# Kernel tuning notes

Measured on AMD Instinct MI355X. Metric: run time of the kernel, lower is better.

Reference implementation:

```python
import jax, jax.numpy as jnp
import numpy as np
from jax import lax

D_TEMPORAL, D_INNER, D_STATE, D_CONV, DT_RANK = 2, 4, 16, 4, 1
EPS = 1e-5


def setup_inputs() -> dict:
    key = jax.random.key(0)
    ks = jax.random.split(key, 14)
    B, L = 16, 32768
    f = lambda k, s, scale=1.0: jax.random.normal(k, s, jnp.float32) * scale
    dt_b = float(np.log(np.expm1(0.01)))  # softplus^-1(0.01), typical dt init
    A_log = jnp.log(jnp.tile(jnp.arange(1, D_STATE + 1, dtype=jnp.float32), (D_INNER, 1)))
    return {
        "hidden_states": f(ks[0], (B, D_TEMPORAL, L)),
        "norm_w": jnp.ones((D_TEMPORAL,), jnp.float32),
        "in_proj_w": f(ks[1], (2 * D_INNER, D_TEMPORAL), 0.5),
        "conv_w": f(ks[2], (D_INNER, D_CONV), 0.3),
        "conv_b": f(ks[3], (D_INNER,), 0.1),
        "x_proj_w": f(ks[4], (DT_RANK + 2 * D_STATE, D_INNER), 0.3),
        "dt_proj_w": f(ks[5], (D_INNER, DT_RANK), 1.0),
        "dt_proj_b": jnp.full((D_INNER,), dt_b, jnp.float32),
        "A_log": A_log,
        "D": jnp.ones((D_INNER,), jnp.float32),
        "conv_w_b": f(ks[6], (D_INNER, D_CONV), 0.3),
        "conv_b_b": f(ks[7], (D_INNER,), 0.1),
        "x_proj_w_b": f(ks[8], (DT_RANK + 2 * D_STATE, D_INNER), 0.3),
        "dt_proj_w_b": f(ks[9], (D_INNER, DT_RANK), 1.0),
        "dt_proj_b_b": jnp.full((D_INNER,), dt_b, jnp.float32),
        "A_b_log": A_log,
        "D_b": jnp.ones((D_INNER,), jnp.float32),
        "out_proj_w": f(ks[10], (D_TEMPORAL, D_INNER), 0.3),
        "norm_f_w": jnp.ones((D_TEMPORAL,), jnp.float32),
    }


def _silu(x):
    return x * jax.nn.sigmoid(x)


def _rmsnorm(x, w):
    return x * lax.rsqrt(jnp.mean(x * x, axis=-1, keepdims=True) + EPS) * w


def _branch(x, z, conv_w, conv_b, x_proj_w, dt_proj_w, dt_proj_b, A_log, D):
    # x, z: (B, d_inner, L). Causal depthwise conv + silu.
    Bb, d, L = x.shape
    xc = lax.conv_general_dilated(
        x, conv_w[:, None, :], (1,), [(D_CONV - 1, 0)],
        feature_group_count=d, dimension_numbers=("NCH", "OIH", "NCH"))
    u = _silu(xc + conv_b[None, :, None]).transpose(0, 2, 1)      # (B, L, d)
    x_dbl = u @ x_proj_w.T                                        # (B, L, rank+2n)
    dt, Bm, Cm = jnp.split(x_dbl, [DT_RANK, DT_RANK + D_STATE], axis=-1)
    dt = jax.nn.softplus(dt @ dt_proj_w.T + dt_proj_b)            # (B, L, d)
    A = -jnp.exp(A_log)                                           # (d, n)
    dA = jnp.exp(dt[..., None] * A)                               # (B, L, d, n)
    dBu = (dt * u)[..., None] * Bm[:, :, None, :]                 # (B, L, d, n)

    def step(h, inp):
        dA_t, dBu_t, C_t = inp
        h = dA_t * h + dBu_t                                      # (B, d, n)
        return h, jnp.einsum("bdn,bn->bd", h, C_t)

    h0 = jnp.zeros((Bb, d, D_STATE), dtype=u.dtype)
    _, ys = lax.scan(step, h0, (jnp.swapaxes(dA, 0, 1), jnp.swapaxes(dBu, 0, 1), jnp.swapaxes(Cm, 0, 1)))
    y = jnp.swapaxes(ys, 0, 1) + u * D                            # (B, L, d)
    return y * _silu(z.transpose(0, 2, 1))


def _forward(hidden_states, norm_w, in_proj_w, conv_w, conv_b, x_proj_w, dt_proj_w,
             dt_proj_b, A_log, D, conv_w_b, conv_b_b, x_proj_w_b, dt_proj_w_b,
             dt_proj_b_b, A_b_log, D_b, out_proj_w, norm_f_w):
    # hidden_states: (B, T=d_temporal, L); scan runs over L.
    hs = jnp.swapaxes(hidden_states, 1, 2)                        # (B, L, T)
    residual = hs.astype(jnp.float32)
    hs = _rmsnorm(residual, norm_w)
    xz = jnp.swapaxes(hs @ in_proj_w.T, 1, 2)                     # (B, 2*d_inner, L)
    x, z = jnp.split(xz, 2, axis=1)
    y_f = _branch(x, z, conv_w, conv_b, x_proj_w, dt_proj_w, dt_proj_b, A_log, D)
    y_b = _branch(x[..., ::-1], z[..., ::-1], conv_w_b, conv_b_b, x_proj_w_b,
                  dt_proj_w_b, dt_proj_b_b, A_b_log, D_b)
    y = y_f + y_b[:, ::-1, :]                                     # (B, L, d_inner)
    out = y @ out_proj_w.T                                        # (B, L, T)
    out = _rmsnorm(out + residual, norm_f_w)
    return jnp.swapaxes(out, 1, 2)                                # (B, T, L)


def reference(hidden_states, norm_w, in_proj_w, conv_w, conv_b, x_proj_w, dt_proj_w,
              dt_proj_b, A_log, D, conv_w_b, conv_b_b, x_proj_w_b, dt_proj_w_b,
              dt_proj_b_b, A_b_log, D_b, out_proj_w, norm_f_w):
    return _forward(hidden_states, norm_w, in_proj_w, conv_w, conv_b, x_proj_w,
                    dt_proj_w, dt_proj_b, A_log, D, conv_w_b, conv_b_b, x_proj_w_b,
                    dt_proj_w_b, dt_proj_b_b, A_b_log, D_b, out_proj_w, norm_f_w)
```

## Files before the change

### kernel.cpp

```cpp
#include <hip/hip_runtime.h>
#include <cstdint>

#define BB 16
#define LL 32768
#define NC 512

#define WD_SZ 256
#define XPW 0
#define CVW 132
#define CVB 148
#define DTW 152
#define DTB 156
#define AW  160
#define DW  224
#define G_INPROJ 512
#define G_NORMW 528
#define G_OUTP 530
#define G_NORMF 538
#define FLG 1000

#define PQ_OFF 4096
#define PQ_BYTES ((size_t)BB*2*NC*64*8)
#define HIN_OFF (PQ_OFF + PQ_BYTES)

__device__ __forceinline__ float bf2f(unsigned short u){ return __uint_as_float(((unsigned int)u)<<16); }
__device__ __forceinline__ float blo(unsigned int u){ return __uint_as_float(u<<16); }
__device__ __forceinline__ float bhi(unsigned int u){ return __uint_as_float(u & 0xffff0000u); }
__device__ __forceinline__ unsigned short f2bf(float f){
  unsigned int x = __float_as_uint(f);
  x += 0x7fffu + ((x>>16)&1u);
  return (unsigned short)(x>>16);
}
__device__ __forceinline__ unsigned int pack2(float a, float b){
  return (unsigned int)f2bf(a) | ((unsigned int)f2bf(b)<<16);
}
__device__ __forceinline__ float siluf(float x){ return x / (1.f + __expf(-x)); }
__device__ __forceinline__ float softplusf_(float x){ return fmaxf(x,0.f) + log1pf(__expf(-fabsf(x))); }

__device__ __forceinline__ float rowsum16(float x){
  union { float f; int i; } a, t;
  a.f = x;
  t.i = __builtin_amdgcn_update_dpp(0, a.i, 0x121, 0xf, 0xf, true); a.f += t.f;
  t.i = __builtin_amdgcn_update_dpp(0, a.i, 0x122, 0xf, 0xf, true); a.f += t.f;
  t.i = __builtin_amdgcn_update_dpp(0, a.i, 0x124, 0xf, 0xf, true); a.f += t.f;
  t.i = __builtin_amdgcn_update_dpp(0, a.i, 0x128, 0xf, 0xf, true); a.f += t.f;
  return a.f;
}

__device__ __forceinline__ float ldw(const void* p, int i, int isf){
  return isf ? ((const float*)p)[i] : bf2f(((const unsigned short*)p)[i]);
}
__device__ __forceinline__ float2 hid2(const void* hid, int isf, int b, int t){
  if (isf){
    const float* p = (const float*)hid;
    return make_float2(p[(size_t)b*2*LL + t], p[(size_t)b*2*LL + LL + t]);
  }
  const unsigned short* p = (const unsigned short*)hid;
  return make_float2(bf2f(p[(size_t)b*2*LL + t]), bf2f(p[(size_t)b*2*LL + LL + t]));
}
__device__ __forceinline__ float4 xrow(const void* __restrict__ hid, int isf,
                                       const float* __restrict__ W, int b, int t){
  float2 h = hid2(hid, isf, b, t);
  float ms = rsqrtf(0.5f*(h.x*h.x + h.y*h.y) + 1e-5f);
  float v0 = h.x*ms*W[G_NORMW], v1 = h.y*ms*W[G_NORMW+1];
  float4 x;
  x.x = W[G_INPROJ+0]*v0 + W[G_INPROJ+1]*v1;
  x.y = W[G_INPROJ+2]*v0 + W[G_INPROJ+3]*v1;
  x.z = W[G_INPROJ+4]*v0 + W[G_INPROJ+5]*v1;
  x.w = W[G_INPROJ+6]*v0 + W[G_INPROJ+7]*v1;
  return x;
}

__global__ void k_prep(const void* __restrict__ normw, const void* __restrict__ inpj,
    const void* __restrict__ cwf, const void* __restrict__ cbf,
    const void* __restrict__ xpf, const void* __restrict__ dwf,
    const void* __restrict__ dbf, const void* __restrict__ alf,
    const void* __restrict__ ddf,
    const void* __restrict__ cwb, const void* __restrict__ cbb,
    const void* __restrict__ xpb, const void* __restrict__ dwb,
    const void* __restrict__ dbb, const void* __restrict__ alb,
    const void* __restrict__ ddb,
    const void* __restrict__ outp, const void* __restrict__ nfw,
    float* __restrict__ W)
{
  const int isf = (((const unsigned int*)ddf)[0] == 0x3F800000u) ? 1 : 0;
  int t = threadIdx.x;
  for (int i=t;i<132;i+=256){ W[XPW+i]=ldw(xpf,i,isf); W[WD_SZ+XPW+i]=ldw(xpb,i,isf); }
  for (int i=t;i<16;i+=256){ W[CVW+i]=ldw(cwf,i,isf); W[WD_SZ+CVW+i]=ldw(cwb,i,isf); W[G_INPROJ+i]=ldw(inpj,i,isf); }
  for (int i=t;i<4;i+=256){
    W[CVB+i]=ldw(cbf,i,isf); W[WD_SZ+CVB+i]=ldw(cbb,i,isf);
    W[DTW+i]=ldw(dwf,i,isf); W[WD_SZ+DTW+i]=ldw(dwb,i,isf);
    W[DTB+i]=ldw(dbf,i,isf); W[WD_SZ+DTB+i]=ldw(dbb,i,isf);
    W[DW+i] =ldw(ddf,i,isf); W[WD_SZ+DW+i] =ldw(ddb,i,isf);
  }
  for (int i=t;i<64;i+=256){ W[AW+i] = -__expf(ldw(alf,i,isf)); W[WD_SZ+AW+i] = -__expf(ldw(alb,i,isf)); }
  for (int i=t;i<8;i+=256) W[G_OUTP+i]=ldw(outp,i,isf);
  for (int i=t;i<2;i+=256){ W[G_NORMW+i]=ldw(normw,i,isf); W[G_NORMF+i]=ldw(nfw,i,isf); }
  if (t==0) W[FLG] = (float)isf;
}

__global__ __launch_bounds__(64) void k_chunk(const void* __restrict__ hid,
    const float* __restrict__ W, float2* __restrict__ PQ)
{
  __shared__ __align__(16) float4 xb[70];
  __shared__ __align__(16) float dtP[2][4][68];
  __shared__ __align__(16) unsigned short dtuP[2][4][72];
  __shared__ __align__(16) unsigned short Bp[2][16][72];
  const int lane = threadIdx.x;
  const int gid  = blockIdx.x;
  const int c    = gid & (NC-1);
  const int b    = gid >> 9;
  const int isf  = (int)W[FLG];

  {
    int t = c*64 + lane;
    xb[lane+3] = xrow(hid, isf, W, b, t);
    if (lane < 3){
      int t2 = c*64 - 3 + lane;
      float4 v = make_float4(0.f,0.f,0.f,0.f);
      if (t2 >= 0) v = xrow(hid, isf, W, b, t2);
      xb[lane] = v;
    }
    if (lane >= 61){
      int t3 = c*64 + lane + 3;
      float4 v = make_float4(0.f,0.f,0.f,0.f);
      if (t3 < LL) v = xrow(hid, isf, W, b, t3);
      xb[lane+6] = v;
    }
  }
  __syncthreads();
  {
    float4 xk0=xb[lane],xk1=xb[lane+1],xk2=xb[lane+2],xk3=xb[lane+3];
    float4 xk4=xb[lane+4],xk5=xb[lane+5],xk6=xb[lane+6];
    float uf[4], ub[4];
    uf[0] = siluf(W[CVB+0] + W[CVW+ 0]*xk0.x + W[CVW+ 1]*xk1.x + W[CVW+ 2]*xk2.x + W[CVW+ 3]*xk3.x);
    uf[1] = siluf(W[CVB+1] + W[CVW+ 4]*xk0.y + W[CVW+ 5]*xk1.y + W[CVW+ 6]*xk2.y + W[CVW+ 7]*xk3.y);
    uf[2] = siluf(W[CVB+2] + W[CVW+ 8]*xk0.z + W[CVW+ 9]*xk1.z + W[CVW+10]*xk2.z + W[CVW+11]*xk3.z);
    uf[3] = siluf(W[CVB+3] + W[CVW+12]*xk0.w + W[CVW+13]*xk1.w + W[CVW+14]*xk2.w + W[CVW+15]*xk3.w);
    const float* Wb = W + WD_SZ;
    ub[0] = siluf(Wb[CVB+0] + Wb[CVW+ 0]*xk6.x + Wb[CVW+ 1]*xk5.x + Wb[CVW+ 2]*xk4.x + Wb[CVW+ 3]*xk3.x);
    ub[1] = siluf(Wb[CVB+1] + Wb[CVW+ 4]*xk6.y + Wb[CVW+ 5]*xk5.y + Wb[CVW+ 6]*xk4.y + Wb[CVW+ 7]*xk3.y);
    ub[2] = siluf(Wb[CVB+2] + Wb[CVW+ 8]*xk6.z + Wb[CVW+ 9]*xk5.z + Wb[CVW+10]*xk4.z + Wb[CVW+11]*xk3.z);
    ub[3] = siluf(Wb[CVB+3] + Wb[CVW+12]*xk6.w + Wb[CVW+13]*xk5.w + Wb[CVW+14]*xk4.w + Wb[CVW+15]*xk3.w);
    #pragma unroll
    for (int dr=0; dr<2; dr++){
      const float* Wd = W + dr*WD_SZ;
      const float* uu = dr ? ub : uf;
      float dtr = Wd[XPW+0]*uu[0] + Wd[XPW+1]*uu[1] + Wd[XPW+2]*uu[2] + Wd[XPW+3]*uu[3];
      #pragma unroll
      for (int d2=0; d2<4; d2++){
        float dt = softplusf_(fmaf(Wd[DTW+d2], dtr, Wd[DTB+d2]));
        dtP[dr][d2][lane]  = dt;
        dtuP[dr][d2][lane] = f2bf(dt*uu[d2]);
      }
      #pragma unroll
      for (int n=0; n<16; n++){
        float Bn = Wd[XPW+(1+n)*4+0]*uu[0] + Wd[XPW+(1+n)*4+1]*uu[1]
                 + Wd[XPW+(1+n)*4+2]*uu[2] + Wd[XPW+(1+n)*4+3]*uu[3];
        Bp[dr][n][lane] = f2bf(Bn);
      }
    }
  }
  __syncthreads();
  const int d = lane>>4, n = lane&15;
  const float Af = W[AW + d*16 + n];
  const float Ab = W[WD_SZ + AW + d*16 + n];
  float Pf=1.f, Qf=0.f, Pb=1.f, Qb=0.f;
  for (int j4=0; j4<16; j4++){
    const int t0f = j4*4, t0b = 60 - j4*4;
    float4 df4 = *(const float4*)&dtP[0][d][t0f];
    float4 db4 = *(const float4*)&dtP[1][d][t0b];
    ushort4 uf4 = *(const ushort4*)&dtuP[0][d][t0f];
    ushort4 ub4 = *(const ushort4*)&dtuP[1][d][t0b];
    ushort4 bf4 = *(const ushort4*)&Bp[0][n][t0f];
    ushort4 bb4 = *(const ushort4*)&Bp[1][n][t0b];
    float dfa[4]={df4.x,df4.y,df4.z,df4.w}, dba[4]={db4.x,db4.y,db4.z,db4.w};
    unsigned short ufa[4]={uf4.x,uf4.y,uf4.z,uf4.w}, uba[4]={ub4.x,ub4.y,ub4.z,ub4.w};
    unsigned short bfa[4]={bf4.x,bf4.y,bf4.z,bf4.w}, bba[4]={bb4.x,bb4.y,bb4.z,bb4.w};
    #pragma unroll
    for (int jr=0; jr<4; jr++){
      float e = __expf(Af*dfa[jr]);
      Pf *= e;
      Qf = fmaf(Qf, e, bf2f(ufa[jr])*bf2f(bfa[jr]));
      const int k = 3-jr;
      float eb = __expf(Ab*dba[k]);
      Pb *= eb;
      Qb = fmaf(Qb, eb, bf2f(uba[k])*bf2f(bba[k]));
    }
  }
  PQ[((size_t)(b*2+0)*NC + c)*64 + lane]          = make_float2(Pf,Qf);
  PQ[((size_t)(b*2+1)*NC + (NC-1-c))*64 + lane]   = make_float2(Pb,Qb);
}

__global__ __launch_bounds__(64) void k_scan(const float2* __restrict__ PQ, float* __restrict__ hin)
{
  int bd = blockIdx.x; int lane = threadIdx.x;
  float h = 0.f;
  size_t base = (size_t)bd*NC;
  for (int c0=0; c0<NC; c0+=16){
    float2 v[16];
    #pragma unroll
    for (int k=0;k<16;k++) v[k] = PQ[(base+c0+k)*64 + lane];
    #pragma unroll
    for (int k=0;k<16;k++){
      hin[(base+c0+k)*64 + lane] = h;
      h = fmaf(v[k].x, h, v[k].y);
    }
  }
}

__global__ __launch_bounds__(64) void k_fused(const void* __restrict__ hid,
    const float* __restrict__ W, const float* __restrict__ hin,
    void* __restrict__ out)
{
  __shared__ __align__(16) float4 xb[70];
  __shared__ __align__(16) float dtP[2][4][68];
  __shared__ __align__(16) unsigned short dtuP[2][4][72];
  __shared__ __align__(16) unsigned int BCp[2][16][68];
  __shared__ __align__(16) float ySf[4][68];
  __shared__ __align__(16) float ySb[4][68];
  __shared__ __align__(16) float zs[256];
  __shared__ __align__(16) float uD2[2][256];
  const int lane = threadIdx.x;
  const int gid  = blockIdx.x;
  const int c    = gid & (NC-1);
  const int b    = gid >> 9;
  const int isf  = (int)W[FLG];

  float hF = hin[((size_t)(b*2+0)*NC + c)*64 + lane];
  float hB = hin[((size_t)(b*2+1)*NC + (NC-1-c))*64 + lane];

  {
    int t = c*64 + lane;
    float2 h = hid2(hid, isf, b, t);
    float ms = rsqrtf(0.5f*(h.x*h.x + h.y*h.y) + 1e-5f);
    float v0 = h.x*ms*W[G_NORMW], v1 = h.y*ms*W[G_NORMW+1];
    float4 x;
    x.x = W[G_INPROJ+0]*v0 + W[G_INPROJ+1]*v1;
    x.y = W[G_INPROJ+2]*v0 + W[G_INPROJ+3]*v1;
    x.z = W[G_INPROJ+4]*v0 + W[G_INPROJ+5]*v1;
    x.w = W[G_INPROJ+6]*v0 + W[G_INPROJ+7]*v1;
    xb[lane+3] = x;
    float4 z4;
    z4.x = siluf(W[G_INPROJ+ 8]*v0 + W[G_INPROJ+ 9]*v1);
    z4.y = siluf(W[G_INPROJ+10]*v0 + W[G_INPROJ+11]*v1);
    z4.z = siluf(W[G_INPROJ+12]*v0 + W[G_INPROJ+13]*v1);
    z4.w = siluf(W[G_INPROJ+14]*v0 + W[G_INPROJ+15]*v1);
    *(float4*)&zs[lane*4] = z4;
    if (lane < 3){
      int t2 = c*64 - 3 + lane;
      float4 v = make_float4(0.f,0.f,0.f,0.f);
      if (t2 >= 0) v = xrow(hid, isf, W, b, t2);
      xb[lane] = v;
    }
    if (lane >= 61){
      int t3 = c*64 + lane + 3;
      float4 v = make_float4(0.f,0.f,0.f,0.f);
      if (t3 < LL) v = xrow(hid, isf, W, b, t3);
      xb[lane+6] = v;
    }
  }
  __syncthreads();
  {
    float4 xk0=xb[lane],xk1=xb[lane+1],xk2=xb[lane+2],xk3=xb[lane+3];
    float4 xk4=xb[lane+4],xk5=xb[lane+5],xk6=xb[lane+6];
    float uf[4], ub[4];
    uf[0] = siluf(W[CVB+0] + W[CVW+ 0]*xk0.x + W[CVW+ 1]*xk1.x + W[CVW+ 2]*xk2.x + W[CVW+ 3]*xk3.x);
    uf[1] = siluf(W[CVB+1] + W[CVW+ 4]*xk0.y + W[CVW+ 5]*xk1.y + W[CVW+ 6]*xk2.y + W[CVW+ 7]*xk3.y);
    uf[2] = siluf(W[CVB+2] + W[CVW+ 8]*xk0.z + W[CVW+ 9]*xk1.z + W[CVW+10]*xk2.z + W[CVW+11]*xk3.z);
    uf[3] = siluf(W[CVB+3] + W[CVW+12]*xk0.w + W[CVW+13]*xk1.w + W[CVW+14]*xk2.w + W[CVW+15]*xk3.w);
    const float* Wb = W + WD_SZ;
    ub[0] = siluf(Wb[CVB+0] + Wb[CVW+ 0]*xk6.x + Wb[CVW+ 1]*xk5.x + Wb[CVW+ 2]*xk4.x + Wb[CVW+ 3]*xk3.x);
    ub[1] = siluf(Wb[CVB+1] + Wb[CVW+ 4]*xk6.y + Wb[CVW+ 5]*xk5.y + Wb[CVW+ 6]*xk4.y + Wb[CVW+ 7]*xk3.y);
    ub[2] = siluf(Wb[CVB+2] + Wb[CVW+ 8]*xk6.z + Wb[CVW+ 9]*xk5.z + Wb[CVW+10]*xk4.z + Wb[CVW+11]*xk3.z);
    ub[3] = siluf(Wb[CVB+3] + Wb[CVW+12]*xk6.w + Wb[CVW+13]*xk5.w + Wb[CVW+14]*xk4.w + Wb[CVW+15]*xk3.w);
    #pragma unroll
    for (int dr=0; dr<2; dr++){
      const float* Wd = W + dr*WD_SZ;
      const float* uu = dr ? ub : uf;
      float dtr = Wd[XPW+0]*uu[0] + Wd[XPW+1]*uu[1] + Wd[XPW+2]*uu[2] + Wd[XPW+3]*uu[3];
      float4 ud4;
      #pragma unroll
      for (int d2=0; d2<4; d2++){
        float dt = softplusf_(fmaf(Wd[DTW+d2], dtr, Wd[DTB+d2]));
        dtP[dr][d2][lane]  = dt;
        dtuP[dr][d2][lane] = f2bf(dt*uu[d2]);
        ((float*)&ud4)[d2] = uu[d2]*Wd[DW+d2];
      }
      *(float4*)&uD2[dr][lane*4] = ud4;
      #pragma unroll
      for (int n=0; n<16; n++){
        float Bn = Wd[XPW+(1+n)*4+0]*uu[0] + Wd[XPW+(1+n)*4+1]*uu[1]
                 + Wd[XPW+(1+n)*4+2]*uu[2] + Wd[XPW+(1+n)*4+3]*uu[3];
        float Cn = Wd[XPW+(17+n)*4+0]*uu[0] + Wd[XPW+(17+n)*4+1]*uu[1]
                 + Wd[XPW+(17+n)*4+2]*uu[2] + Wd[XPW+(17+n)*4+3]*uu[3];
        BCp[dr][n][lane] = pack2(Bn, Cn);
      }
    }
  }
  __syncthreads();

  const int d = lane>>4, n = lane&15;
  const float Af = W[AW + d*16 + n];
  const float Ab = W[WD_SZ + AW + d*16 + n];
  for (int j4=0; j4<16; j4++){
    const int t0f = j4*4, t0b = 60 - j4*4;
    float4 df4 = *(const float4*)&dtP[0][d][t0f];
    float4 db4 = *(const float4*)&dtP[1][d][t0b];
    ushort4 uf4 = *(const ushort4*)&dtuP[0][d][t0f];
    ushort4 ub4 = *(const ushort4*)&dtuP[1][d][t0b];
    uint4 cf4 = *(const uint4*)&BCp[0][n][t0f];
    uint4 cb4 = *(const uint4*)&BCp[1][n][t0b];
    float dfa[4]={df4.x,df4.y,df4.z,df4.w}, dba[4]={db4.x,db4.y,db4.z,db4.w};
    unsigned short ufa[4]={uf4.x,uf4.y,uf4.z,uf4.w}, uba[4]={ub4.x,ub4.y,ub4.z,ub4.w};
    unsigned int cfa[4]={cf4.x,cf4.y,cf4.z,cf4.w}, cba[4]={cb4.x,cb4.y,cb4.z,cb4.w};
    float sF[4], sB[4];
    #pragma unroll
    for (int jr=0; jr<4; jr++){
      float e = __expf(Af*dfa[jr]);
      hF = fmaf(e, hF, bf2f(ufa[jr])*blo(cfa[jr]));
      sF[jr] = rowsum16(hF*bhi(cfa[jr]));
      const int k = 3-jr;
      float eb = __expf(Ab*dba[k]);
      hB = fmaf(eb, hB, bf2f(uba[k])*blo(cba[k]));
      sB[k] = rowsum16(hB*bhi(cba[k]));
    }
    if (n == 0){
      *(float4*)&ySf[d][t0f] = make_float4(sF[0],sF[1],sF[2],sF[3]);
      *(float4*)&ySb[d][t0b] = make_float4(sB[0],sB[1],sB[2],sB[3]);
    }
  }
  __syncthreads();

  {
    int t = c*64 + lane;
    float4 zz = *(const float4*)&zs[lane*4];
    float4 u0 = *(const float4*)&uD2[0][lane*4];
    float4 u1 = *(const float4*)&uD2[1][lane*4];
    float y0 = (ySf[0][lane] + ySb[0][lane] + u0.x + u1.x) * zz.x;
    float y1 = (ySf[1][lane] + ySb[1][lane] + u0.y + u1.y) * zz.y;
    float y2 = (ySf[2][lane] + ySb[2][lane] + u0.z + u1.z) * zz.z;
    float y3 = (ySf[3][lane] + ySb[3][lane] + u0.w + u1.w) * zz.w;
    float o0 = W[G_OUTP+0]*y0 + W[G_OUTP+1]*y1 + W[G_OUTP+2]*y2 + W[G_OUTP+3]*y3;
    float o1 = W[G_OUTP+4]*y0 + W[G_OUTP+5]*y1 + W[G_OUTP+6]*y2 + W[G_OUTP+7]*y3;
    float2 r = hid2(hid, isf, b, t);
    o0 += r.x;
    o1 += r.y;
    float ms = rsqrtf(0.5f*(o0*o0 + o1*o1) + 1e-5f);
    float e0 = o0*ms*W[G_NORMF], e1 = o1*ms*W[G_NORMF+1];
    size_t i0 = (size_t)b*2*LL + t, i1 = i0 + LL;
    if (isf){
      ((float*)out)[i0] = e0;
      ((float*)out)[i1] = e1;
    } else {
      ((unsigned short*)out)[i0] = f2bf(e0);
      ((unsigned short*)out)[i1] = f2bf(e1);
    }
  }
}

extern "C" void kernel_launch(void* const* d_in, const int* in_sizes, int n_in,
                              void* d_out, int out_size, void* d_ws, size_t ws_size,
                              hipStream_t stream)
{
  (void)in_sizes; (void)n_in; (void)out_size; (void)ws_size;
  const void* hid   = d_in[0];
  const void* normw = d_in[1];
  const void* inpj  = d_in[2];
  const void* cwf   = d_in[3];
  const void* cbf   = d_in[4];
  const void* xpf   = d_in[5];
  const void* dwf   = d_in[6];
  const void* dbf   = d_in[7];
  const void* alf   = d_in[8];
  const void* ddf   = d_in[9];
  const void* cwb   = d_in[10];
  const void* cbb   = d_in[11];
  const void* xpb   = d_in[12];
  const void* dwb   = d_in[13];
  const void* dbb   = d_in[14];
  const void* alb   = d_in[15];
  const void* ddb   = d_in[16];
  const void* outp  = d_in[17];
  const void* nfw   = d_in[18];

  float* W   = (float*)d_ws;
  float2* PQ = (float2*)((char*)d_ws + PQ_OFF);
  float* hin = (float*)((char*)d_ws + HIN_OFF);

  k_prep<<<1,256,0,stream>>>(normw, inpj, cwf, cbf, xpf, dwf, dbf, alf, ddf,
                             cwb, cbb, xpb, dwb, dbb, alb, ddb, outp, nfw, W);
  k_chunk<<<BB*NC, 64, 0, stream>>>(hid, W, PQ);
  k_scan<<<BB*2, 64, 0, stream>>>(PQ, hin);
  k_fused<<<BB*NC, 64, 0, stream>>>(hid, W, hin, d_out);
}
```

Baseline: 206.9 us.

## Share precomputed chunk planes between passes and split the carry scan across four waves

The chunk pass now writes its per-chunk dt, dt*u, packed B/C, z and D*u planes to workspace, so the fused pass can load them instead of recomputing conv, projections and activations. This applies only when the workspace is large enough; otherwise both passes recompute as before. The carry scan now runs four waves per sequence, each over its own segment, then corrects the carries with the prefix of the earlier segments. Silu and softplus use cheaper hardware rcp and log2 intrinsics. The cost is about 109 MB of extra global write and read traffic.

```diff
diff --git a/kernel.cpp b/kernel.cpp
--- a/kernel.cpp
+++ b/kernel.cpp
@@ -22,6 +22,11 @@
 #define PQ_OFF 4096
 #define PQ_BYTES ((size_t)BB*2*NC*64*8)
 #define HIN_OFF (PQ_OFF + PQ_BYTES)
+#define HIN_BYTES ((size_t)BB*2*NC*64*4)
+#define PLN_OFF (HIN_OFF + HIN_BYTES)
+#define PLN_STRIDE 13312
+#define PLN_BYTES ((size_t)BB*NC*PLN_STRIDE)
+
 
 __device__ __forceinline__ float bf2f(unsigned short u){ return __uint_as_float(((unsigned int)u)<<16); }
 __device__ __forceinline__ float blo(unsigned int u){ return __uint_as_float(u<<16); }
@@ -34,8 +39,12 @@
 __device__ __forceinline__ unsigned int pack2(float a, float b){
   return (unsigned int)f2bf(a) | ((unsigned int)f2bf(b)<<16);
 }
-__device__ __forceinline__ float siluf(float x){ return x / (1.f + __expf(-x)); }
-__device__ __forceinline__ float softplusf_(float x){ return fmaxf(x,0.f) + log1pf(__expf(-fabsf(x))); }
+__device__ __forceinline__ float siluf(float x){
+  return x * __builtin_amdgcn_rcpf(1.f + __expf(-x));
+}
+__device__ __forceinline__ float softplusf_(float x){
+  return fmaxf(x,0.f) + 0.69314718056f*__log2f(1.f + __expf(-fabsf(x)));
+}
 
 __device__ __forceinline__ float rowsum16(float x){
   union { float f; int i; } a, t;
@@ -71,165 +80,18 @@
   return x;
 }
 
-__global__ void k_prep(const void* __restrict__ normw, const void* __restrict__ inpj,
-    const void* __restrict__ cwf, const void* __restrict__ cbf,
-    const void* __restrict__ xpf, const void* __restrict__ dwf,
-    const void* __restrict__ dbf, const void* __restrict__ alf,
-    const void* __restrict__ ddf,
-    const void* __restrict__ cwb, const void* __restrict__ cbb,
-    const void* __restrict__ xpb, const void* __restrict__ dwb,
-    const void* __restrict__ dbb, const void* __restrict__ alb,
-    const void* __restrict__ ddb,
-    const void* __restrict__ outp, const void* __restrict__ nfw,
-    float* __restrict__ W)
-{
-  const int isf = (((const unsigned int*)ddf)[0] == 0x3F800000u) ? 1 : 0;
-  int t = threadIdx.x;
-  for (int i=t;i<132;i+=256){ W[XPW+i]=ldw(xpf,i,isf); W[WD_SZ+XPW+i]=ldw(xpb,i,isf); }
-  for (int i=t;i<16;i+=256){ W[CVW+i]=ldw(cwf,i,isf); W[WD_SZ+CVW+i]=ldw(cwb,i,isf); W[G_INPROJ+i]=ldw(inpj,i,isf); }
-  for (int i=t;i<4;i+=256){
-    W[CVB+i]=ldw(cbf,i,isf); W[WD_SZ+CVB+i]=ldw(cbb,i,isf);
-    W[DTW+i]=ldw(dwf,i,isf); W[WD_SZ+DTW+i]=ldw(dwb,i,isf);
-    W[DTB+i]=ldw(dbf,i,isf); W[WD_SZ+DTB+i]=ldw(dbb,i,isf);
-    W[DW+i] =ldw(ddf,i,isf); W[WD_SZ+DW+i] =ldw(ddb,i,isf);
-  }
-  for (int i=t;i<64;i+=256){ W[AW+i] = -__expf(ldw(alf,i,isf)); W[WD_SZ+AW+i] = -__expf(ldw(alb,i,isf)); }
-  for (int i=t;i<8;i+=256) W[G_OUTP+i]=ldw(outp,i,isf);
-  for (int i=t;i<2;i+=256){ W[G_NORMW+i]=ldw(normw,i,isf); W[G_NORMF+i]=ldw(nfw,i,isf); }
-  if (t==0) W[FLG] = (float)isf;
-}
-
-__global__ __launch_bounds__(64) void k_chunk(const void* __restrict__ hid,
-    const float* __restrict__ W, float2* __restrict__ PQ)
-{
-  __shared__ __align__(16) float4 xb[70];
-  __shared__ __align__(16) float dtP[2][4][68];
-  __shared__ __align__(16) unsigned short dtuP[2][4][72];
-  __shared__ __align__(16) unsigned short Bp[2][16][72];
-  const int lane = threadIdx.x;
-  const int gid  = blockIdx.x;
-  const int c    = gid & (NC-1);
-  const int b    = gid >> 9;
-  const int isf  = (int)W[FLG];
-
-  {
-    int t = c*64 + lane;
-    xb[lane+3] = xrow(hid, isf, W, b, t);
-    if (lane < 3){
-      int t2 = c*64 - 3 + lane;
-      float4 v = make_float4(0.f,0.f,0.f,0.f);
-      if (t2 >= 0) v = xrow(hid, isf, W, b, t2);
-      xb[lane] = v;
-    }
-    if (lane >= 61){
-      int t3 = c*64 + lane + 3;
-      float4 v = make_float4(0.f,0.f,0.f,0.f);
-      if (t3 < LL) v = xrow(hid, isf, W, b, t3);
-      xb[lane+6] = v;
-    }
-  }
-  __syncthreads();
-  {
-    float4 xk0=xb[lane],xk1=xb[lane+1],xk2=xb[lane+2],xk3=xb[lane+3];
-    float4 xk4=xb[lane+4],xk5=xb[lane+5],xk6=xb[lane+6];
-    float uf[4], ub[4];
-    uf[0] = siluf(W[CVB+0] + W[CVW+ 0]*xk0.x + W[CVW+ 1]*xk1.x + W[CVW+ 2]*xk2.x + W[CVW+ 3]*xk3.x);
-    uf[1] = siluf(W[CVB+1] + W[CVW+ 4]*xk0.y + W[CVW+ 5]*xk1.y + W[CVW+ 6]*xk2.y + W[CVW+ 7]*xk3.y);
-    uf[2] = siluf(W[CVB+2] + W[CVW+ 8]*xk0.z + W[CVW+ 9]*xk1.z + W[CVW+10]*xk2.z + W[CVW+11]*xk3.z);
-    uf[3] = siluf(W[CVB+3] + W[CVW+12]*xk0.w + W[CVW+13]*xk1.w + W[CVW+14]*xk2.w + W[CVW+15]*xk3.w);
-    const float* Wb = W + WD_SZ;
-    ub[0] = siluf(Wb[CVB+0] + Wb[CVW+ 0]*xk6.x + Wb[CVW+ 1]*xk5.x + Wb[CVW+ 2]*xk4.x + Wb[CVW+ 3]*xk3.x);
-    ub[1] = siluf(Wb[CVB+1] + Wb[CVW+ 4]*xk6.y + Wb[CVW+ 5]*xk5.y + Wb[CVW+ 6]*xk4.y + Wb[CVW+ 7]*xk3.y);
-    ub[2] = siluf(Wb[CVB+2] + Wb[CVW+ 8]*xk6.z + Wb[CVW+ 9]*xk5.z + Wb[CVW+10]*xk4.z + Wb[CVW+11]*xk3.z);
-    ub[3] = siluf(Wb[CVB+3] + Wb[CVW+12]*xk6.w + Wb[CVW+13]*xk5.w + Wb[CVW+14]*xk4.w + Wb[CVW+15]*xk3.w);
-    #pragma unroll
-    for (int dr=0; dr<2; dr++){
-      const float* Wd = W + dr*WD_SZ;
-      const float* uu = dr ? ub : uf;
-      float dtr = Wd[XPW+0]*uu[0] + Wd[XPW+1]*uu[1] + Wd[XPW+2]*uu[2] + Wd[XPW+3]*uu[3];
-      #pragma unroll
-      for (int d2=0; d2<4; d2++){
-        float dt = softplusf_(fmaf(Wd[DTW+d2], dtr, Wd[DTB+d2]));
-        dtP[dr][d2][lane]  = dt;
-        dtuP[dr][d2][lane] = f2bf(dt*uu[d2]);
-      }
-      #pragma unroll
-      for (int n=0; n<16; n++){
-        float Bn = Wd[XPW+(1+n)*4+0]*uu[0] + Wd[XPW+(1+n)*4+1]*uu[1]
-                 + Wd[XPW+(1+n)*4+2]*uu[2] + Wd[XPW+(1+n)*4+3]*uu[3];
-        Bp[dr][n][lane] = f2bf(Bn);
-      }
-    }
-  }
-  __syncthreads();
-  const int d = lane>>4, n = lane&15;
-  const float Af = W[AW + d*16 + n];
-  const float Ab = W[WD_SZ + AW + d*16 + n];
-  float Pf=1.f, Qf=0.f, Pb=1.f, Qb=0.f;
-  for (int j4=0; j4<16; j4++){
-    const int t0f = j4*4, t0b = 60 - j4*4;
-    float4 df4 = *(const float4*)&dtP[0][d][t0f];
-    float4 db4 = *(const float4*)&dtP[1][d][t0b];
-    ushort4 uf4 = *(const ushort4*)&dtuP[0][d][t0f];
-    ushort4 ub4 = *(const ushort4*)&dtuP[1][d][t0b];
-    ushort4 bf4 = *(const ushort4*)&Bp[0][n][t0f];
-    ushort4 bb4 = *(const ushort4*)&Bp[1][n][t0b];
-    float dfa[4]={df4.x,df4.y,df4.z,df4.w}, dba[4]={db4.x,db4.y,db4.z,db4.w};
-    unsigned short ufa[4]={uf4.x,uf4.y,uf4.z,uf4.w}, uba[4]={ub4.x,ub4.y,ub4.z,ub4.w};
-    unsigned short bfa[4]={bf4.x,bf4.y,bf4.z,bf4.w}, bba[4]={bb4.x,bb4.y,bb4.z,bb4.w};
-    #pragma unroll
-    for (int jr=0; jr<4; jr++){
-      float e = __expf(Af*dfa[jr]);
-      Pf *= e;
-      Qf = fmaf(Qf, e, bf2f(ufa[jr])*bf2f(bfa[jr]));
-      const int k = 3-jr;
-      float eb = __expf(Ab*dba[k]);
-      Pb *= eb;
-      Qb = fmaf(Qb, eb, bf2f(uba[k])*bf2f(bba[k]));
-    }
-  }
-  PQ[((size_t)(b*2+0)*NC + c)*64 + lane]          = make_float2(Pf,Qf);
-  PQ[((size_t)(b*2+1)*NC + (NC-1-c))*64 + lane]   = make_float2(Pb,Qb);
-}
-
-__global__ __launch_bounds__(64) void k_scan(const float2* __restrict__ PQ, float* __restrict__ hin)
-{
-  int bd = blockIdx.x; int lane = threadIdx.x;
-  float h = 0.f;
-  size_t base = (size_t)bd*NC;
-  for (int c0=0; c0<NC; c0+=16){
-    float2 v[16];
-    #pragma unroll
-    for (int k=0;k<16;k++) v[k] = PQ[(base+c0+k)*64 + lane];
-    #pragma unroll
-    for (int k=0;k<16;k++){
-      hin[(base+c0+k)*64 + lane] = h;
-      h = fmaf(v[k].x, h, v[k].y);
-    }
-  }
-}
-
-__global__ __launch_bounds__(64) void k_fused(const void* __restrict__ hid,
-    const float* __restrict__ W, const float* __restrict__ hin,
-    void* __restrict__ out)
-{
-  __shared__ __align__(16) float4 xb[70];
-  __shared__ __align__(16) float dtP[2][4][68];
-  __shared__ __align__(16) unsigned short dtuP[2][4][72];
-  __shared__ __align__(16) unsigned int BCp[2][16][68];
-  __shared__ __align__(16) float ySf[4][68];
-  __shared__ __align__(16) float ySb[4][68];
-  __shared__ __align__(16) float zs[256];
-  __shared__ __align__(16) float uD2[2][256];
-  const int lane = threadIdx.x;
-  const int gid  = blockIdx.x;
-  const int c    = gid & (NC-1);
-  const int b    = gid >> 9;
-  const int isf  = (int)W[FLG];
-
-  float hF = hin[((size_t)(b*2+0)*NC + c)*64 + lane];
-  float hB = hin[((size_t)(b*2+1)*NC + (NC-1-c))*64 + lane];
-
+__device__ __forceinline__ void phaseA(const void* __restrict__ hid, int isf,
+    const float* __restrict__ W, int b, int c, int lane,
+    unsigned char* smem, float4* xb)
+{
+  float* dtF = (float*)(smem);
+  float* dtB = (float*)(smem+1024);
+  unsigned short* duF = (unsigned short*)(smem+2048);
+  unsigned short* duB = (unsigned short*)(smem+2560);
+  unsigned int* BCF = (unsigned int*)(smem+3072);
+  unsigned int* BCB = (unsigned int*)(smem+7168);
+  float* zsP = (float*)(smem+11264);
+  float* uDP = (float*)(smem+12288);
   {
     int t = c*64 + lane;
     float2 h = hid2(hid, isf, b, t);
@@ -246,7 +108,7 @@
     z4.y = siluf(W[G_INPROJ+10]*v0 + W[G_INPROJ+11]*v1);
     z4.z = siluf(W[G_INPROJ+12]*v0 + W[G_INPROJ+13]*v1);
     z4.w = siluf(W[G_INPROJ+14]*v0 + W[G_INPROJ+15]*v1);
-    *(float4*)&zs[lane*4] = z4;
+    *(float4*)&zsP[lane*4] = z4;
     if (lane < 3){
       int t2 = c*64 - 3 + lane;
       float4 v = make_float4(0.f,0.f,0.f,0.f);
@@ -261,68 +123,237 @@
     }
   }
   __syncthreads();
-  {
-    float4 xk0=xb[lane],xk1=xb[lane+1],xk2=xb[lane+2],xk3=xb[lane+3];
-    float4 xk4=xb[lane+4],xk5=xb[lane+5],xk6=xb[lane+6];
-    float uf[4], ub[4];
-    uf[0] = siluf(W[CVB+0] + W[CVW+ 0]*xk0.x + W[CVW+ 1]*xk1.x + W[CVW+ 2]*xk2.x + W[CVW+ 3]*xk3.x);
-    uf[1] = siluf(W[CVB+1] + W[CVW+ 4]*xk0.y + W[CVW+ 5]*xk1.y + W[CVW+ 6]*xk2.y + W[CVW+ 7]*xk3.y);
-    uf[2] = siluf(W[CVB+2] + W[CVW+ 8]*xk0.z + W[CVW+ 9]*xk1.z + W[CVW+10]*xk2.z + W[CVW+11]*xk3.z);
-    uf[3] = siluf(W[CVB+3] + W[CVW+12]*xk0.w + W[CVW+13]*xk1.w + W[CVW+14]*xk2.w + W[CVW+15]*xk3.w);
-    const float* Wb = W + WD_SZ;
-    ub[0] = siluf(Wb[CVB+0] + Wb[CVW+ 0]*xk6.x + Wb[CVW+ 1]*xk5.x + Wb[CVW+ 2]*xk4.x + Wb[CVW+ 3]*xk3.x);
-    ub[1] = siluf(Wb[CVB+1] + Wb[CVW+ 4]*xk6.y + Wb[CVW+ 5]*xk5.y + Wb[CVW+ 6]*xk4.y + Wb[CVW+ 7]*xk3.y);
-    ub[2] = siluf(Wb[CVB+2] + Wb[CVW+ 8]*xk6.z + Wb[CVW+ 9]*xk5.z + Wb[CVW+10]*xk4.z + Wb[CVW+11]*xk3.z);
-    ub[3] = siluf(Wb[CVB+3] + Wb[CVW+12]*xk6.w + Wb[CVW+13]*xk5.w + Wb[CVW+14]*xk4.w + Wb[CVW+15]*xk3.w);
-    #pragma unroll
-    for (int dr=0; dr<2; dr++){
-      const float* Wd = W + dr*WD_SZ;
-      const float* uu = dr ? ub : uf;
-      float dtr = Wd[XPW+0]*uu[0] + Wd[XPW+1]*uu[1] + Wd[XPW+2]*uu[2] + Wd[XPW+3]*uu[3];
-      float4 ud4;
+  float4 xk0=xb[lane],xk1=xb[lane+1],xk2=xb[lane+2],xk3=xb[lane+3];
+  float4 xk4=xb[lane+4],xk5=xb[lane+5],xk6=xb[lane+6];
+  float uf[4], ub[4];
+  uf[0] = siluf(W[CVB+0] + W[CVW+ 0]*xk0.x + W[CVW+ 1]*xk1.x + W[CVW+ 2]*xk2.x + W[CVW+ 3]*xk3.x);
+  uf[1] = siluf(W[CVB+1] + W[CVW+ 4]*xk0.y + W[CVW+ 5]*xk1.y + W[CVW+ 6]*xk2.y + W[CVW+ 7]*xk3.y);
+  uf[2] = siluf(W[CVB+2] + W[CVW+ 8]*xk0.z + W[CVW+ 9]*xk1.z + W[CVW+10]*xk2.z + W[CVW+11]*xk3.z);
+  uf[3] = siluf(W[CVB+3] + W[CVW+12]*xk0.w + W[CVW+13]*xk1.w + W[CVW+14]*xk2.w + W[CVW+15]*xk3.w);
+  const float* Wb = W + WD_SZ;
+  ub[0] = siluf(Wb[CVB+0] + Wb[CVW+ 0]*xk6.x + Wb[CVW+ 1]*xk5.x + Wb[CVW+ 2]*xk4.x + Wb[CVW+ 3]*xk3.x);
+  ub[1] = siluf(Wb[CVB+1] + Wb[CVW+ 4]*xk6.y + Wb[CVW+ 5]*xk5.y + Wb[CVW+ 6]*xk4.y + Wb[CVW+ 7]*xk3.y);
+  ub[2] = siluf(Wb[CVB+2] + Wb[CVW+ 8]*xk6.z + Wb[CVW+ 9]*xk5.z + Wb[CVW+10]*xk4.z + Wb[CVW+11]*xk3.z);
+  ub[3] = siluf(Wb[CVB+3] + Wb[CVW+12]*xk6.w + Wb[CVW+13]*xk5.w + Wb[CVW+14]*xk4.w + Wb[CVW+15]*xk3.w);
+  *(float4*)&uDP[lane*4] = make_float4(
+      uf[0]*W[DW+0]+ub[0]*Wb[DW+0], uf[1]*W[DW+1]+ub[1]*Wb[DW+1],
+      uf[2]*W[DW+2]+ub[2]*Wb[DW+2], uf[3]*W[DW+3]+ub[3]*Wb[DW+3]);
+  #pragma unroll
+  for (int dr=0; dr<2; dr++){
+    const float* Wd = W + dr*WD_SZ;
+    const float* uu = dr ? ub : uf;
+    float* dtp = dr ? dtB : dtF;
+    unsigned short* dup = dr ? duB : duF;
+    unsigned int* bcp = dr ? BCB : BCF;
+    float dtr = Wd[XPW+0]*uu[0]+Wd[XPW+1]*uu[1]+Wd[XPW+2]*uu[2]+Wd[XPW+3]*uu[3];
+    #pragma unroll
+    for (int d2=0; d2<4; d2++){
+      float dt = softplusf_(fmaf(Wd[DTW+d2], dtr, Wd[DTB+d2]));
+      dtp[d2*64+lane] = dt;
+      dup[d2*64+lane] = f2bf(dt*uu[d2]);
+    }
+    #pragma unroll
+    for (int n=0;n<16;n++){
+      float Bn = Wd[XPW+(1+n)*4+0]*uu[0]+Wd[XPW+(1+n)*4+1]*uu[1]
+               + Wd[XPW+(1+n)*4+2]*uu[2]+Wd[XPW+(1+n)*4+3]*uu[3];
+      float Cn = Wd[XPW+(17+n)*4+0]*uu[0]+Wd[XPW+(17+n)*4+1]*uu[1]
+               + Wd[XPW+(17+n)*4+2]*uu[2]+Wd[XPW+(17+n)*4+3]*uu[3];
+      bcp[n*64+lane] = pack2(Bn,Cn);
+    }
+  }
+}
+
+__global__ void k_prep(const void* __restrict__ normw, const void* __restrict__ inpj,
+    const void* __restrict__ cwf, const void* __restrict__ cbf,
+    const void* __restrict__ xpf, const void* __restrict__ dwf,
+    const void* __restrict__ dbf, const void* __restrict__ alf,
+    const void* __restrict__ ddf,
+    const void* __restrict__ cwb, const void* __restrict__ cbb,
+    const void* __restrict__ xpb, const void* __restrict__ dwb,
+    const void* __restrict__ dbb, const void* __restrict__ alb,
+    const void* __restrict__ ddb,
+    const void* __restrict__ outp, const void* __restrict__ nfw,
+    float* __restrict__ W)
+{
+  const int isf = (((const unsigned int*)ddf)[0] == 0x3F800000u) ? 1 : 0;
+  int t = threadIdx.x;
+  for (int i=t;i<132;i+=256){ W[XPW+i]=ldw(xpf,i,isf); W[WD_SZ+XPW+i]=ldw(xpb,i,isf); }
+  for (int i=t;i<16;i+=256){ W[CVW+i]=ldw(cwf,i,isf); W[WD_SZ+CVW+i]=ldw(cwb,i,isf); W[G_INPROJ+i]=ldw(inpj,i,isf); }
+  for (int i=t;i<4;i+=256){
+    W[CVB+i]=ldw(cbf,i,isf); W[WD_SZ+CVB+i]=ldw(cbb,i,isf);
+    W[DTW+i]=ldw(dwf,i,isf); W[WD_SZ+DTW+i]=ldw(dwb,i,isf);
+    W[DTB+i]=ldw(dbf,i,isf); W[WD_SZ+DTB+i]=ldw(dbb,i,isf);
+    W[DW+i] =ldw(ddf,i,isf); W[WD_SZ+DW+i] =ldw(ddb,i,isf);
+  }
+  for (int i=t;i<64;i+=256){ W[AW+i] = -__expf(ldw(alf,i,isf)); W[WD_SZ+AW+i] = -__expf(ldw(alb,i,isf)); }
+  for (int i=t;i<8;i+=256) W[G_OUTP+i]=ldw(outp,i,isf);
+  for (int i=t;i<2;i+=256){ W[G_NORMW+i]=ldw(normw,i,isf); W[G_NORMF+i]=ldw(nfw,i,isf); }
+  if (t==0) W[FLG] = (float)isf;
+}
+
+template<bool SPL>
+__global__ __launch_bounds__(64) void k_chunk(const void* __restrict__ hid,
+    const float* __restrict__ W, float2* __restrict__ PQ,
+    unsigned char* __restrict__ planes)
+{
+  __shared__ __align__(16) unsigned char smem[13312];
+  __shared__ __align__(16) float4 xb[70];
+  const int lane = threadIdx.x;
+  const int gid  = blockIdx.x;
+  const int c    = gid & (NC-1);
+  const int b    = gid >> 9;
+  const int isf  = (int)W[FLG];
+
+  phaseA(hid, isf, W, b, c, lane, smem, xb);
+  __syncthreads();
+  if (SPL){
+    uint4* gp = (uint4*)(planes + (size_t)gid*PLN_STRIDE);
+    const uint4* sp = (const uint4*)smem;
+    #pragma unroll
+    for (int i=0;i<13;i++) gp[i*64+lane] = sp[i*64+lane];
+  }
+  const float* dtF = (const float*)(smem);
+  const float* dtB = (const float*)(smem+1024);
+  const unsigned short* duF = (const unsigned short*)(smem+2048);
+  const unsigned short* duB = (const unsigned short*)(smem+2560);
+  const unsigned int* BCF = (const unsigned int*)(smem+3072);
+  const unsigned int* BCB = (const unsigned int*)(smem+7168);
+  const int d = lane>>4, n = lane&15;
+  const float Af = W[AW + d*16 + n];
+  const float Ab = W[WD_SZ + AW + d*16 + n];
+  float Pf=1.f, Qf=0.f, Pb=1.f, Qb=0.f;
+  for (int j4=0; j4<16; j4++){
+    const int t0f = j4*4, t0b = 60 - j4*4;
+    float4 df4 = *(const float4*)&dtF[d*64+t0f];
+    float4 db4 = *(const float4*)&dtB[d*64+t0b];
+    uint2 uf2 = *(const uint2*)&duF[d*64+t0f];
+    uint2 ub2 = *(const uint2*)&duB[d*64+t0b];
+    uint4 cf4 = *(const uint4*)&BCF[n*64+t0f];
+    uint4 cb4 = *(const uint4*)&BCB[n*64+t0b];
+    float dfa[4]={df4.x,df4.y,df4.z,df4.w}, dba[4]={db4.x,db4.y,db4.z,db4.w};
+    float duf[4]={blo(uf2.x),bhi(uf2.x),blo(uf2.y),bhi(uf2.y)};
+    float dub[4]={blo(ub2.x),bhi(ub2.x),blo(ub2.y),bhi(ub2.y)};
+    unsigned int cfa[4]={cf4.x,cf4.y,cf4.z,cf4.w}, cba[4]={cb4.x,cb4.y,cb4.z,cb4.w};
+    #pragma unroll
+    for (int jr=0; jr<4; jr++){
+      float e = __expf(Af*dfa[jr]);
+      Pf *= e;
+      Qf = fmaf(Qf, e, duf[jr]*blo(cfa[jr]));
+      const int k = 3-jr;
+      float eb = __expf(Ab*dba[k]);
+      Pb *= eb;
+      Qb = fmaf(Qb, eb, dub[k]*blo(cba[k]));
+    }
+  }
+  PQ[((size_t)(b*2+0)*NC + c)*64 + lane]        = make_float2(Pf,Qf);
+  PQ[((size_t)(b*2+1)*NC + (NC-1-c))*64 + lane] = make_float2(Pb,Qb);
+}
+
+__global__ __launch_bounds__(256) void k_scan(const float2* __restrict__ PQ, float* __restrict__ hin)
+{
+  __shared__ float2 seg[4][64];
+  const int bd = blockIdx.x;
+  const int lane = threadIdx.x & 63;
+  const int w = threadIdx.x >> 6;
+  const size_t base = (size_t)bd*NC;
+  const int c0 = w*128;
+  float h = 0.f, R = 1.f;
+  for (int cc=0; cc<128; cc+=16){
+    float2 v[16];
+    #pragma unroll
+    for (int k=0;k<16;k++) v[k] = PQ[(base+c0+cc+k)*64+lane];
+    #pragma unroll
+    for (int k=0;k<16;k++){
+      hin[(base+c0+cc+k)*64+lane] = h;
+      h = fmaf(v[k].x, h, v[k].y);
+      R *= v[k].x;
+    }
+  }
+  seg[w][lane] = make_float2(R, h);
+  __syncthreads();
+  if (w > 0){
+    float init = 0.f;
+    #pragma unroll
+    for (int s=0; s<3; s++){
+      if (s < w){ float2 pq = seg[s][lane]; init = fmaf(pq.x, init, pq.y); }
+    }
+    float Rr = 1.f;
+    for (int cc=0; cc<128; cc+=16){
+      float pv[16], hv[16];
       #pragma unroll
-      for (int d2=0; d2<4; d2++){
-        float dt = softplusf_(fmaf(Wd[DTW+d2], dtr, Wd[DTB+d2]));
-        dtP[dr][d2][lane]  = dt;
-        dtuP[dr][d2][lane] = f2bf(dt*uu[d2]);
-        ((float*)&ud4)[d2] = uu[d2]*Wd[DW+d2];
+      for (int k=0;k<16;k++) pv[k] = PQ[(base+c0+cc+k)*64+lane].x;
+      #pragma unroll
+      for (int k=0;k<16;k++) hv[k] = hin[(base+c0+cc+k)*64+lane];
+      #pragma unroll
+      for (int k=0;k<16;k++){
+        hin[(base+c0+cc+k)*64+lane] = hv[k] + init*Rr;
+        Rr *= pv[k];
       }
-      *(float4*)&uD2[dr][lane*4] = ud4;
-      #pragma unroll
-      for (int n=0; n<16; n++){
-        float Bn = Wd[XPW+(1+n)*4+0]*uu[0] + Wd[XPW+(1+n)*4+1]*uu[1]
-                 + Wd[XPW+(1+n)*4+2]*uu[2] + Wd[XPW+(1+n)*4+3]*uu[3];
-        float Cn = Wd[XPW+(17+n)*4+0]*uu[0] + Wd[XPW+(17+n)*4+1]*uu[1]
-                 + Wd[XPW+(17+n)*4+2]*uu[2] + Wd[XPW+(17+n)*4+3]*uu[3];
-        BCp[dr][n][lane] = pack2(Bn, Cn);
-      }
-    }
+    }
+  }
+}
+
+template<bool LPL>
+__global__ __launch_bounds__(64) void k_fused(const void* __restrict__ hid,
+    const float* __restrict__ W, const float* __restrict__ hin,
+    const unsigned char* __restrict__ planes, void* __restrict__ out)
+{
+  __shared__ __align__(16) unsigned char smem[13312];
+  __shared__ __align__(16) float ySf[4][68];
+  __shared__ __align__(16) float ySb[4][68];
+  const int lane = threadIdx.x;
+  const int gid  = blockIdx.x;
+  const int c    = gid & (NC-1);
+  const int b    = gid >> 9;
+  const int isf  = (int)W[FLG];
+
+  float hF = hin[((size_t)(b*2+0)*NC + c)*64 + lane];
+  float hB = hin[((size_t)(b*2+1)*NC + (NC-1-c))*64 + lane];
+
+  if constexpr (LPL){
+    const uint4* gp = (const uint4*)(planes + (size_t)gid*PLN_STRIDE);
+    uint4* sp = (uint4*)smem;
+    #pragma unroll
+    for (int i=0;i<13;i++) sp[i*64+lane] = gp[i*64+lane];
+  } else {
+    __shared__ __align__(16) float4 xb[70];
+    phaseA(hid, isf, W, b, c, lane, smem, xb);
   }
   __syncthreads();
+
+  const float* dtF = (const float*)(smem);
+  const float* dtB = (const float*)(smem+1024);
+  const unsigned short* duF = (const unsigned short*)(smem+2048);
+  const unsigned short* duB = (const unsigned short*)(smem+2560);
+  const unsigned int* BCF = (const unsigned int*)(smem+3072);
+  const unsigned int* BCB = (const unsigned int*)(smem+7168);
+  const float* zsP = (const float*)(smem+11264);
+  const float* uDP = (const float*)(smem+12288);
 
   const int d = lane>>4, n = lane&15;
   const float Af = W[AW + d*16 + n];
   const float Ab = W[WD_SZ + AW + d*16 + n];
   for (int j4=0; j4<16; j4++){
     const int t0f = j4*4, t0b = 60 - j4*4;
-    float4 df4 = *(const float4*)&dtP[0][d][t0f];
-    float4 db4 = *(const float4*)&dtP[1][d][t0b];
-    ushort4 uf4 = *(const ushort4*)&dtuP[0][d][t0f];
-    ushort4 ub4 = *(const ushort4*)&dtuP[1][d][t0b];
-    uint4 cf4 = *(const uint4*)&BCp[0][n][t0f];
-    uint4 cb4 = *(const uint4*)&BCp[1][n][t0b];
+    float4 df4 = *(const float4*)&dtF[d*64+t0f];
+    float4 db4 = *(const float4*)&dtB[d*64+t0b];
+    uint2 uf2 = *(const uint2*)&duF[d*64+t0f];
+    uint2 ub2 = *(const uint2*)&duB[d*64+t0b];
+    uint4 cf4 = *(const uint4*)&BCF[n*64+t0f];
+    uint4 cb4 = *(const uint4*)&BCB[n*64+t0b];
     float dfa[4]={df4.x,df4.y,df4.z,df4.w}, dba[4]={db4.x,db4.y,db4.z,db4.w};
-    unsigned short ufa[4]={uf4.x,uf4.y,uf4.z,uf4.w}, uba[4]={ub4.x,ub4.y,ub4.z,ub4.w};
+    float duf[4]={blo(uf2.x),bhi(uf2.x),blo(uf2.y),bhi(uf2.y)};
+    float dub[4]={blo(ub2.x),bhi(ub2.x),blo(ub2.y),bhi(ub2.y)};
     unsigned int cfa[4]={cf4.x,cf4.y,cf4.z,cf4.w}, cba[4]={cb4.x,cb4.y,cb4.z,cb4.w};
     float sF[4], sB[4];
     #pragma unroll
     for (int jr=0; jr<4; jr++){
       float e = __expf(Af*dfa[jr]);
-      hF = fmaf(e, hF, bf2f(ufa[jr])*blo(cfa[jr]));
+      hF = fmaf(e, hF, duf[jr]*blo(cfa[jr]));
       sF[jr] = rowsum16(hF*bhi(cfa[jr]));
       const int k = 3-jr;
       float eb = __expf(Ab*dba[k]);
-      hB = fmaf(eb, hB, bf2f(uba[k])*blo(cba[k]));
+      hB = fmaf(eb, hB, dub[k]*blo(cba[k]));
       sB[k] = rowsum16(hB*bhi(cba[k]));
     }
     if (n == 0){
@@ -331,16 +362,14 @@
     }
   }
   __syncthreads();
-
   {
     int t = c*64 + lane;
-    float4 zz = *(const float4*)&zs[lane*4];
-    float4 u0 = *(const float4*)&uD2[0][lane*4];
-    float4 u1 = *(const float4*)&uD2[1][lane*4];
-    float y0 = (ySf[0][lane] + ySb[0][lane] + u0.x + u1.x) * zz.x;
-    float y1 = (ySf[1][lane] + ySb[1][lane] + u0.y + u1.y) * zz.y;
-    float y2 = (ySf[2][lane] + ySb[2][lane] + u0.z + u1.z) * zz.z;
-    float y3 = (ySf[3][lane] + ySb[3][lane] + u0.w + u1.w) * zz.w;
+    float4 zz = *(const float4*)&zsP[lane*4];
+    float4 ud = *(const float4*)&uDP[lane*4];
+    float y0 = (ySf[0][lane] + ySb[0][lane] + ud.x) * zz.x;
+    float y1 = (ySf[1][lane] + ySb[1][lane] + ud.y) * zz.y;
+    float y2 = (ySf[2][lane] + ySb[2][lane] + ud.z) * zz.z;
+    float y3 = (ySf[3][lane] + ySb[3][lane] + ud.w) * zz.w;
     float o0 = W[G_OUTP+0]*y0 + W[G_OUTP+1]*y1 + W[G_OUTP+2]*y2 + W[G_OUTP+3]*y3;
     float o1 = W[G_OUTP+4]*y0 + W[G_OUTP+5]*y1 + W[G_OUTP+6]*y2 + W[G_OUTP+7]*y3;
     float2 r = hid2(hid, isf, b, t);
@@ -363,34 +392,24 @@
                               void* d_out, int out_size, void* d_ws, size_t ws_size,
                               hipStream_t stream)
 {
-  (void)in_sizes; (void)n_in; (void)out_size; (void)ws_size;
+  (void)in_sizes; (void)n_in; (void)out_size;
   const void* hid   = d_in[0];
-  const void* normw = d_in[1];
-  const void* inpj  = d_in[2];
-  const void* cwf   = d_in[3];
-  const void* cbf   = d_in[4];
-  const void* xpf   = d_in[5];
-  const void* dwf   = d_in[6];
-  const void* dbf   = d_in[7];
-  const void* alf   = d_in[8];
-  const void* ddf   = d_in[9];
-  const void* cwb   = d_in[10];
-  const void* cbb   = d_in[11];
-  const void* xpb   = d_in[12];
-  const void* dwb   = d_in[13];
-  const void* dbb   = d_in[14];
-  const void* alb   = d_in[15];
-  const void* ddb   = d_in[16];
-  const void* outp  = d_in[17];
-  const void* nfw   = d_in[18];
-
   float* W   = (float*)d_ws;
   float2* PQ = (float2*)((char*)d_ws + PQ_OFF);
   float* hin = (float*)((char*)d_ws + HIN_OFF);
-
-  k_prep<<<1,256,0,stream>>>(normw, inpj, cwf, cbf, xpf, dwf, dbf, alf, ddf,
-                             cwb, cbb, xpb, dwb, dbb, alb, ddb, outp, nfw, W);
-  k_chunk<<<BB*NC, 64, 0, stream>>>(hid, W, PQ);
-  k_scan<<<BB*2, 64, 0, stream>>>(PQ, hin);
-  k_fused<<<BB*NC, 64, 0, stream>>>(hid, W, hin, d_out);
-}
+  unsigned char* planes = (unsigned char*)d_ws + PLN_OFF;
+
+  k_prep<<<1,256,0,stream>>>(d_in[1], d_in[2], d_in[3], d_in[4], d_in[5], d_in[6],
+                             d_in[7], d_in[8], d_in[9], d_in[10], d_in[11], d_in[12],
+                             d_in[13], d_in[14], d_in[15], d_in[16], d_in[17], d_in[18], W);
+  const bool useP = ws_size >= (size_t)(PLN_OFF + PLN_BYTES);
+  if (useP){
+    k_chunk<true><<<BB*NC, 64, 0, stream>>>(hid, W, PQ, planes);
+    k_scan<<<BB*2, 256, 0, stream>>>(PQ, hin);
+    k_fused<true><<<BB*NC, 64, 0, stream>>>(hid, W, hin, planes, d_out);
+  } else {
+    k_chunk<false><<<BB*NC, 64, 0, stream>>>(hid, W, PQ, planes);
+    k_scan<<<BB*2, 256, 0, stream>>>(PQ, hin);
+    k_fused<false><<<BB*NC, 64, 0, stream>>>(hid, W, hin, planes, d_out);
+  }
+}
```

Result: slower. 211.4 us (+2.2%).
